# Kernel tuning notes

Measured on AMD Instinct MI355X. Metric: run time of the kernel, lower is better.

The kernel has to match this reference:

```python
import jax, jax.numpy as jnp
import numpy as np

B, I, H, OH = 16384, 256, 256, 64
N_STEPS = 8  # fixed-step dopri5 (adaptive step control replaced by fixed grid for jit)


def setup_inputs() -> dict:
    key = jax.random.key(0)
    ks = jax.random.split(key, 12)
    sH = 1.0 / np.sqrt(H)
    sOH = 1.0 / np.sqrt(OH)
    u = lambda k, shape, s: jax.random.uniform(k, shape, jnp.float32, -s, s)
    return {
        "input": jax.random.normal(ks[0], (B, I), jnp.float32),
        "h_prev": jax.random.normal(ks[1], (B, H), jnp.float32),
        "c_prev": jax.random.normal(ks[2], (B, H), jnp.float32),
        "timespans": jax.random.uniform(ks[3], (B,), jnp.float32, 0.05, 1.0),
        # LSTMCell params (PyTorch layout: gates stacked as [i, f, g, o])
        "W_ih": u(ks[4], (4 * H, I), sH),
        "W_hh": u(ks[5], (4 * H, H), sH),
        "b_ih": u(ks[6], (4 * H,), sH),
        "b_hh": u(ks[7], (4 * H,), sH),
        # ode_func: Linear(H, OH) -> Tanh -> Linear(OH, H)
        "W1": u(ks[8], (OH, H), sH),
        "b1": u(ks[9], (OH,), sH),
        "W2": u(ks[10], (H, OH), sOH),
        "b2": u(ks[11], (H,), sOH),
    }


def reference(input, h_prev, c_prev, timespans, W_ih, W_hh, b_ih, b_hh, W1, b1, W2, b2):
    # --- LSTMCell ---
    gates = input @ W_ih.T + b_ih + h_prev @ W_hh.T + b_hh  # (B, 4H)
    gi, gf, gg, go = jnp.split(gates, 4, axis=-1)
    i = jax.nn.sigmoid(gi)
    f = jax.nn.sigmoid(gf)
    g = jnp.tanh(gg)
    o = jax.nn.sigmoid(go)
    c = f * c_prev + i * g
    h = o * jnp.tanh(c)

    # --- Neural ODE: dy/dt = MLP(y), autonomous, Dormand-Prince RK45 ---
    def ode_f(y):
        return jnp.tanh(y @ W1.T + b1) @ W2.T + b2

    dt = (timespans / N_STEPS)[:, None]  # (B, 1) per-sample step size

    def dopri5_step(y, _):
        k1 = ode_f(y)
        k2 = ode_f(y + dt * (1.0 / 5.0 * k1))
        k3 = ode_f(y + dt * (3.0 / 40.0 * k1 + 9.0 / 40.0 * k2))
        k4 = ode_f(y + dt * (44.0 / 45.0 * k1 - 56.0 / 15.0 * k2 + 32.0 / 9.0 * k3))
        k5 = ode_f(y + dt * (19372.0 / 6561.0 * k1 - 25360.0 / 2187.0 * k2
                             + 64448.0 / 6561.0 * k3 - 212.0 / 729.0 * k4))
        k6 = ode_f(y + dt * (9017.0 / 3168.0 * k1 - 355.0 / 33.0 * k2
                             + 46732.0 / 5247.0 * k3 + 49.0 / 176.0 * k4
                             - 5103.0 / 18656.0 * k5))
        y_next = y + dt * (35.0 / 384.0 * k1 + 500.0 / 1113.0 * k3 + 125.0 / 192.0 * k4
                           - 2187.0 / 6784.0 * k5 + 11.0 / 84.0 * k6)
        return y_next, None

    h_ode, _ = jax.lax.scan(dopri5_step, h, None, length=N_STEPS)
    return h_ode, c
```

## Files before the change

### kernel.cpp

```cpp
#include <hip/hip_runtime.h>
#include <hip/hip_bf16.h>


#define B_N 16384
#define H_N 256

typedef __attribute__((ext_vector_type(8))) short short8;
typedef __attribute__((ext_vector_type(4))) unsigned short u16x4;
typedef __attribute__((ext_vector_type(4))) float f32x4;

__device__ __forceinline__ unsigned short f2bf_s(float x) {
  __hip_bfloat16 h = __float2bfloat16(x);
  return *reinterpret_cast<unsigned short*>(&h);
}

__device__ __forceinline__ short8 pack8f(const float* p) {
  const f32x4 a = *(const f32x4*)p;
  const f32x4 b = *(const f32x4*)(p + 4);
  short8 r;
  r[0] = (short)f2bf_s(a[0]); r[1] = (short)f2bf_s(a[1]);
  r[2] = (short)f2bf_s(a[2]); r[3] = (short)f2bf_s(a[3]);
  r[4] = (short)f2bf_s(b[0]); r[5] = (short)f2bf_s(b[1]);
  r[6] = (short)f2bf_s(b[2]); r[7] = (short)f2bf_s(b[3]);
  return r;
}

__device__ __forceinline__ short8 pack8v(f32x4 a, f32x4 b) {
  short8 r;
  r[0] = (short)f2bf_s(a[0]); r[1] = (short)f2bf_s(a[1]);
  r[2] = (short)f2bf_s(a[2]); r[3] = (short)f2bf_s(a[3]);
  r[4] = (short)f2bf_s(b[0]); r[5] = (short)f2bf_s(b[1]);
  r[6] = (short)f2bf_s(b[2]); r[7] = (short)f2bf_s(b[3]);
  return r;
}

__device__ __forceinline__ float fast_sigmoid(float x) {
  return __builtin_amdgcn_rcpf(1.f + __expf(-x));
}
__device__ __forceinline__ float fast_tanh(float x) {
  float e = __expf(2.f * x);
  return 1.f - 2.f * __builtin_amdgcn_rcpf(e + 1.f);
}

__device__ __forceinline__ void gl_lds16(const void* g, void* l) {
  __builtin_amdgcn_global_load_lds(
      (const __attribute__((address_space(1))) void*)g,
      (__attribute__((address_space(3))) void*)l, 16, 0, 0);
}

__global__ __launch_bounds__(256) void prep_kernel(
    const float* __restrict__ Wih, const float* __restrict__ Whh,
    const float* __restrict__ W1, const float* __restrict__ W2,
    const float* __restrict__ b2,
    unsigned short* __restrict__ wsB, unsigned short* __restrict__ wcB,
    float* __restrict__ uF, unsigned short* __restrict__ w1B,
    unsigned short* __restrict__ w2B) {
  const int bx = blockIdx.x;
  if (bx < 256) {
    int idx = bx * 256 + threadIdx.x;
    int n = idx >> 6, c = idx & 63, k = c * 8;
    const float* src = (k < 256) ? (Wih + (size_t)n * 256 + k)
                                 : (Whh + (size_t)n * 256 + (k - 256));
    *(short8*)(wsB + (size_t)n * 512 + k) = pack8f(src);
  } else if (bx < 272) {
    int idx = (bx - 256) * 256 + threadIdx.x;
    int f = idx >> 6, o = idx & 63;
    float a0 = 0.f, a1 = 0.f, a2 = 0.f, a3 = 0.f;
    for (int h = 0; h < 256; h += 4) {
      a0 = fmaf(W1[f * 256 + h],     W2[h * 64 + o],        a0);
      a1 = fmaf(W1[f * 256 + h + 1], W2[(h + 1) * 64 + o],  a1);
      a2 = fmaf(W1[f * 256 + h + 2], W2[(h + 2) * 64 + o],  a2);
      a3 = fmaf(W1[f * 256 + h + 3], W2[(h + 3) * 64 + o],  a3);
    }
    wcB[f * 64 + o] = f2bf_s((a0 + a1) + (a2 + a3));
  } else if (bx == 272) {
    int f = threadIdx.x;
    if (f < 64) {
      float a0 = 0.f, a1 = 0.f, a2 = 0.f, a3 = 0.f;
      for (int h = 0; h < 256; h += 4) {
        a0 = fmaf(W1[f * 256 + h],     b2[h],     a0);
        a1 = fmaf(W1[f * 256 + h + 1], b2[h + 1], a1);
        a2 = fmaf(W1[f * 256 + h + 2], b2[h + 2], a2);
        a3 = fmaf(W1[f * 256 + h + 3], b2[h + 3], a3);
      }
      uF[f] = (a0 + a1) + (a2 + a3);
    }
  } else if (bx < 281) {
    int idx = (bx - 273) * 256 + threadIdx.x;
    *(short8*)(w1B + (size_t)idx * 8) = pack8f(W1 + (size_t)idx * 8);
  } else {
    int idx = (bx - 281) * 256 + threadIdx.x;
    *(short8*)(w2B + (size_t)idx * 8) = pack8f(W2 + (size_t)idx * 8);
  }
}

__global__ __launch_bounds__(512, 4) void lstm_kernel(
    const float* __restrict__ x, const float* __restrict__ hp,
    const float* __restrict__ cp, const unsigned short* __restrict__ wsB,
    const float* __restrict__ bih, const float* __restrict__ bhh,
    float* __restrict__ out) {
  __shared__ __align__(16) float As2[2][128 * 32];
  __shared__ __align__(16) unsigned short Bs2[2][256 * 32];

  const int tid = threadIdx.x;
  const int lane = tid & 63;
  const int wv = tid >> 6;
  const int rg = wv >> 1;
  const int cg = wv & 1;
  const int s = lane & 15, q = lane >> 4;
  const int mb = blockIdx.x * 128;
  const int hb = blockIdx.y * 64;

  f32x4 acc[2][8];
#pragma unroll
  for (int mt = 0; mt < 2; ++mt)
#pragma unroll
    for (int tn = 0; tn < 8; ++tn) acc[mt][tn] = (f32x4){0.f, 0.f, 0.f, 0.f};

  const int c16a = wv * 2;
  const int rowA0 = c16a * 8 + (lane >> 3);
  const int gcA = (lane & 7) ^ (rowA0 & 7);
  const int rowB0 = c16a * 16 + (lane >> 2);
  const int rowB1 = rowB0 + 16;
  const int gcB0 = (lane & 3) ^ ((rowB0 >> 1) & 3);
  const int gcB1 = (lane & 3) ^ ((rowB1 >> 1) & 3);
  const int grB0 = (rowB0 >> 6) * 256 + hb + (rowB0 & 63);
  const int grB1 = (rowB1 >> 6) * 256 + hb + (rowB1 & 63);

  auto STAGE = [&](int buf, int kt) {
    const float* srcA = (kt < 8) ? x : hp;
    const int kl = (kt * 32) & 255;
    gl_lds16(srcA + (size_t)(mb + rowA0) * 256 + kl + gcA * 4,
             (char*)As2[buf] + c16a * 1024);
    gl_lds16(srcA + (size_t)(mb + rowA0 + 8) * 256 + kl + gcA * 4,
             (char*)As2[buf] + (c16a + 1) * 1024);
    gl_lds16(wsB + (size_t)grB0 * 512 + kt * 32 + gcB0 * 8,
             (char*)Bs2[buf] + c16a * 1024);
    gl_lds16(wsB + (size_t)grB1 * 512 + kt * 32 + gcB1 * 8,
             (char*)Bs2[buf] + (c16a + 1) * 1024);
  };

  STAGE(0, 0);
  __syncthreads();

  for (int kt = 0; kt < 16; ++kt) {
    const int buf = kt & 1;
    if (kt < 15) STAGE(buf ^ 1, kt + 1);

    short8 af[2];
#pragma unroll
    for (int mt = 0; mt < 2; ++mt) {
      const int ar = rg * 32 + mt * 16 + s;
      const char* ap = (const char*)As2[buf] + ar * 128;
      float tmp[8];
      *(f32x4*)tmp = *(const f32x4*)(ap + (((q * 2) ^ (ar & 7)) << 4));
      *(f32x4*)(tmp + 4) = *(const f32x4*)(ap + (((q * 2 + 1) ^ (ar & 7)) << 4));
      af[mt] = pack8f(tmp);
    }
    const char* bp = (const char*)Bs2[buf];
#pragma unroll
    for (int tn = 0; tn < 8; ++tn) {
      const int t = (tn >> 1) * 64 + cg * 32 + (tn & 1) * 16 + s;
      short8 bfr = *(const short8*)(bp + t * 64 + ((q ^ ((t >> 1) & 3)) << 4));
      acc[0][tn] = __builtin_amdgcn_mfma_f32_16x16x32_bf16(af[0], bfr, acc[0][tn], 0, 0, 0);
      acc[1][tn] = __builtin_amdgcn_mfma_f32_16x16x32_bf16(af[1], bfr, acc[1][tn], 0, 0, 0);
    }
    __syncthreads();
  }

#pragma unroll
  for (int mt = 0; mt < 2; ++mt)
#pragma unroll
    for (int ntl = 0; ntl < 2; ++ntl)
#pragma unroll
      for (int r = 0; r < 4; ++r) {
        int sample = mb + rg * 32 + mt * 16 + q * 4 + r;
        int h = hb + cg * 32 + ntl * 16 + s;
        float gi = acc[mt][0 + ntl][r] + bih[h] + bhh[h];
        float gf = acc[mt][2 + ntl][r] + bih[256 + h] + bhh[256 + h];
        float gg = acc[mt][4 + ntl][r] + bih[512 + h] + bhh[512 + h];
        float go = acc[mt][6 + ntl][r] + bih[768 + h] + bhh[768 + h];
        float iv = fast_sigmoid(gi), fv = fast_sigmoid(gf);
        float gv = fast_tanh(gg), ov = fast_sigmoid(go);
        float c = fv * cp[(size_t)sample * 256 + h] + iv * gv;
        float hv = ov * fast_tanh(c);
        out[(size_t)B_N * H_N + (size_t)sample * 256 + h] = c;
        out[(size_t)sample * 256 + h] = hv;
      }
}

__global__ __launch_bounds__(64) void ode_kernel(
    float* __restrict__ out, const float* __restrict__ ts,
    const unsigned short* __restrict__ wcB, const float* __restrict__ uF,
    const unsigned short* __restrict__ w1B, const unsigned short* __restrict__ w2B,
    const float* __restrict__ b1, const float* __restrict__ b2) {
  const int lane = threadIdx.x;
  const int s = lane & 15, q = lane >> 4;
  const int bb = blockIdx.x * 16;

  auto grow = [&](int i) {
    return (i >> 1) * 32 + ((s >> 2) * 8) + (i & 1) * 4 + (s & 3);
  };
  auto fbase = [&](int i) { return (i >> 1) * 32 + q * 8 + (i & 1) * 4; };

  short8 wcf[4][2];
#pragma unroll
  for (int i = 0; i < 4; ++i) {
    const int gr = grow(i);
#pragma unroll
    for (int kt = 0; kt < 2; ++kt)
      wcf[i][kt] = *(const short8*)(wcB + (size_t)gr * 64 + kt * 32 + q * 8);
  }
  f32x4 b1v[4], u4[4];
#pragma unroll
  for (int i = 0; i < 4; ++i) {
    b1v[i] = *(const f32x4*)(b1 + fbase(i));
    u4[i] = *(const f32x4*)(uF + fbase(i));
  }
  const float dt = ts[bb + s] * 0.125f;

  f32x4 G[4];
#pragma unroll
  for (int i = 0; i < 4; ++i) G[i] = (f32x4){0.f, 0.f, 0.f, 0.f};
#pragma unroll
  for (int kt = 0; kt < 8; ++kt) {
    short8 yf = pack8f(out + (size_t)(bb + s) * 256 + kt * 32 + q * 8);
#pragma unroll
    for (int i = 0; i < 4; ++i) {
      short8 w1f =
          *(const short8*)(w1B + (size_t)grow(i) * 256 + kt * 32 + q * 8);
      G[i] = __builtin_amdgcn_mfma_f32_16x16x32_bf16(w1f, yf, G[i], 0, 0, 0);
    }
  }

  auto wcmm = [&](const f32x4 (&zc)[4], f32x4 (&o)[4]) {
    short8 zf0 = pack8v(zc[0], zc[1]);
    short8 zf1 = pack8v(zc[2], zc[3]);
#pragma unroll
    for (int i = 0; i < 4; ++i) {
      f32x4 a = (f32x4){0.f, 0.f, 0.f, 0.f};
      a = __builtin_amdgcn_mfma_f32_16x16x32_bf16(wcf[i][0], zf0, a, 0, 0, 0);
      a = __builtin_amdgcn_mfma_f32_16x16x32_bf16(wcf[i][1], zf1, a, 0, 0, 0);
      o[i] = a;
    }
  };
  auto stage = [&](const f32x4 (&zc)[4], float cj, f32x4 (&zo)[4]) {
    f32x4 o[4];
    wcmm(zc, o);
#pragma unroll
    for (int i = 0; i < 4; ++i)
#pragma unroll
      for (int r = 0; r < 4; ++r)
        zo[i][r] =
            fast_tanh(fmaf(dt, fmaf(cj, u4[i][r], o[i][r]), G[i][r]) + b1v[i][r]);
  };

  const float A31 = 3.f / 40.f, A32 = 9.f / 40.f;
  const float A41 = 44.f / 45.f, A42 = -56.f / 15.f, A43 = 32.f / 9.f;
  const float A51 = 19372.f / 6561.f, A52 = -25360.f / 2187.f,
              A53 = 64448.f / 6561.f, A54 = -212.f / 729.f;
  const float A61 = 9017.f / 3168.f, A62 = -355.f / 33.f, A63 = 46732.f / 5247.f,
              A64 = 49.f / 176.f, A65 = -5103.f / 18656.f;
  const float C1 = 35.f / 384.f, C3 = 500.f / 1113.f, C4 = 125.f / 192.f,
              C5 = -2187.f / 6784.f, C6 = 11.f / 84.f;

  f32x4 SC[4];
#pragma unroll
  for (int i = 0; i < 4; ++i) SC[i] = (f32x4){0.f, 0.f, 0.f, 0.f};
  f32x4 z1[4], z2[4], z3[4], z4[4], z5[4], zc[4];

  for (int st = 0; st < 8; ++st) {
#pragma unroll
    for (int i = 0; i < 4; ++i)
#pragma unroll
      for (int r = 0; r < 4; ++r) z1[i][r] = fast_tanh(G[i][r] + b1v[i][r]);

#pragma unroll
    for (int i = 0; i < 4; ++i) zc[i] = 0.2f * z1[i];
    stage(zc, 0.2f, z2);
#pragma unroll
    for (int i = 0; i < 4; ++i) zc[i] = A31 * z1[i] + A32 * z2[i];
    stage(zc, 0.3f, z3);
#pragma unroll
    for (int i = 0; i < 4; ++i) zc[i] = A41 * z1[i] + A42 * z2[i] + A43 * z3[i];
    stage(zc, 0.8f, z4);
#pragma unroll
    for (int i = 0; i < 4; ++i)
      zc[i] = A51 * z1[i] + A52 * z2[i] + A53 * z3[i] + A54 * z4[i];
    stage(zc, 8.f / 9.f, z5);
#pragma unroll
    for (int i = 0; i < 4; ++i)
      zc[i] = A61 * z1[i] + A62 * z2[i] + A63 * z3[i] + A64 * z4[i] + A65 * z5[i];
    {
      f32x4 o[4];
      wcmm(zc, o);
#pragma unroll
      for (int i = 0; i < 4; ++i)
#pragma unroll
        for (int r = 0; r < 4; ++r) {
          float z6v =
              fast_tanh(fmaf(dt, u4[i][r] + o[i][r], G[i][r]) + b1v[i][r]);
          zc[i][r] = C1 * z1[i][r] + C3 * z3[i][r] + C4 * z4[i][r] +
                     C5 * z5[i][r] + C6 * z6v;
        }
    }
    {
      f32x4 o6[4];
      wcmm(zc, o6);
#pragma unroll
      for (int i = 0; i < 4; ++i) {
        SC[i] += zc[i];
#pragma unroll
        for (int r = 0; r < 4; ++r)
          G[i][r] = fmaf(dt, u4[i][r] + o6[i][r], G[i][r]);
      }
    }
  }

  {
    short8 sf0 = pack8v(SC[0], SC[1]);
    short8 sf1 = pack8v(SC[2], SC[3]);
#pragma unroll
    for (int ft = 0; ft < 16; ++ft) {
      short8 w2a = *(const short8*)(w2B + (size_t)(ft * 16 + s) * 64 + q * 8);
      short8 w2b = *(const short8*)(w2B + (size_t)(ft * 16 + s) * 64 + 32 + q * 8);
      f32x4 a = (f32x4){0.f, 0.f, 0.f, 0.f};
      a = __builtin_amdgcn_mfma_f32_16x16x32_bf16(w2a, sf0, a, 0, 0, 0);
      a = __builtin_amdgcn_mfma_f32_16x16x32_bf16(w2b, sf1, a, 0, 0, 0);
      f32x4 y0 = *(const f32x4*)(out + (size_t)(bb + s) * 256 + ft * 16 + q * 4);
      f32x4 b2v = *(const f32x4*)(b2 + ft * 16 + q * 4);
#pragma unroll
      for (int r = 0; r < 4; ++r)
        y0[r] = fmaf(dt, fmaf(8.f, b2v[r], a[r]), y0[r]);
      *(f32x4*)(out + (size_t)(bb + s) * 256 + ft * 16 + q * 4) = y0;
    }
  }
}

extern "C" void kernel_launch(void* const* d_in, const int* in_sizes, int n_in,
                              void* d_out, int out_size, void* d_ws, size_t ws_size,
                              hipStream_t stream) {
  const float* x   = (const float*)d_in[0];
  const float* hp  = (const float*)d_in[1];
  const float* cp  = (const float*)d_in[2];
  const float* ts  = (const float*)d_in[3];
  const float* Wih = (const float*)d_in[4];
  const float* Whh = (const float*)d_in[5];
  const float* bih = (const float*)d_in[6];
  const float* bhh = (const float*)d_in[7];
  const float* W1  = (const float*)d_in[8];
  const float* b1  = (const float*)d_in[9];
  const float* W2  = (const float*)d_in[10];
  const float* b2  = (const float*)d_in[11];
  float* out = (float*)d_out;

  unsigned short* wsB = (unsigned short*)d_ws;
  unsigned short* wcB = (unsigned short*)((char*)d_ws + 1048576);
  float* uF = (float*)((char*)d_ws + 1048576 + 8192);
  unsigned short* w1B = (unsigned short*)((char*)d_ws + 1048576 + 16384);
  unsigned short* w2B = (unsigned short*)((char*)d_ws + 1048576 + 49152);

  prep_kernel<<<289, 256, 0, stream>>>(Wih, Whh, W1, W2, b2, wsB, wcB, uF, w1B, w2B);
  lstm_kernel<<<dim3(128, 4), 512, 0, stream>>>(x, hp, cp, wsB, bih, bhh, out);
  ode_kernel<<<1024, 64, 0, stream>>>(out, ts, wcB, uF, w1B, w2B, b1, b2);
}
```

Measured before the change: 80.73 us.

## Drop LDS staging in LSTM GEMM and halve ODE samples per wave

The LSTM GEMM no longer stages tiles through LDS with double buffering. Each wave now loads A and B fragments straight from global memory and holds a 64x32 tile across all four gates, so the grid shrinks to 256 blocks. The ODE kernel processes 8 samples per 64-lane wave instead of 16, using clamped duplicate lanes and a masked store, which doubles the block count. It also folds b1 into G once rather than adding it in every stage. The trade-off is more redundant global traffic and duplicated MFMA work in exchange for more parallelism and fewer syncs.

```diff
diff --git a/kernel.cpp b/kernel.cpp
--- a/kernel.cpp
+++ b/kernel.cpp
@@ -40,12 +40,6 @@
 __device__ __forceinline__ float fast_tanh(float x) {
   float e = __expf(2.f * x);
   return 1.f - 2.f * __builtin_amdgcn_rcpf(e + 1.f);
-}
-
-__device__ __forceinline__ void gl_lds16(const void* g, void* l) {
-  __builtin_amdgcn_global_load_lds(
-      (const __attribute__((address_space(1))) void*)g,
-      (__attribute__((address_space(3))) void*)l, 16, 0, 0);
 }
 
 __global__ __launch_bounds__(256) void prep_kernel(
@@ -94,92 +88,54 @@
   }
 }
 
-__global__ __launch_bounds__(512, 4) void lstm_kernel(
+__global__ __launch_bounds__(512, 2) void lstm_kernel(
     const float* __restrict__ x, const float* __restrict__ hp,
     const float* __restrict__ cp, const unsigned short* __restrict__ wsB,
     const float* __restrict__ bih, const float* __restrict__ bhh,
     float* __restrict__ out) {
-  __shared__ __align__(16) float As2[2][128 * 32];
-  __shared__ __align__(16) unsigned short Bs2[2][256 * 32];
-
   const int tid = threadIdx.x;
   const int lane = tid & 63;
   const int wv = tid >> 6;
-  const int rg = wv >> 1;
-  const int cg = wv & 1;
   const int s = lane & 15, q = lane >> 4;
-  const int mb = blockIdx.x * 128;
-  const int hb = blockIdx.y * 64;
-
-  f32x4 acc[2][8];
-#pragma unroll
-  for (int mt = 0; mt < 2; ++mt)
+  const int mb = blockIdx.x * 64;
+  const int hb = wv * 32;
+
+  f32x4 acc[4][8];
+#pragma unroll
+  for (int mt = 0; mt < 4; ++mt)
 #pragma unroll
     for (int tn = 0; tn < 8; ++tn) acc[mt][tn] = (f32x4){0.f, 0.f, 0.f, 0.f};
 
-  const int c16a = wv * 2;
-  const int rowA0 = c16a * 8 + (lane >> 3);
-  const int gcA = (lane & 7) ^ (rowA0 & 7);
-  const int rowB0 = c16a * 16 + (lane >> 2);
-  const int rowB1 = rowB0 + 16;
-  const int gcB0 = (lane & 3) ^ ((rowB0 >> 1) & 3);
-  const int gcB1 = (lane & 3) ^ ((rowB1 >> 1) & 3);
-  const int grB0 = (rowB0 >> 6) * 256 + hb + (rowB0 & 63);
-  const int grB1 = (rowB1 >> 6) * 256 + hb + (rowB1 & 63);
-
-  auto STAGE = [&](int buf, int kt) {
+  for (int kt = 0; kt < 16; ++kt) {
     const float* srcA = (kt < 8) ? x : hp;
     const int kl = (kt * 32) & 255;
-    gl_lds16(srcA + (size_t)(mb + rowA0) * 256 + kl + gcA * 4,
-             (char*)As2[buf] + c16a * 1024);
-    gl_lds16(srcA + (size_t)(mb + rowA0 + 8) * 256 + kl + gcA * 4,
-             (char*)As2[buf] + (c16a + 1) * 1024);
-    gl_lds16(wsB + (size_t)grB0 * 512 + kt * 32 + gcB0 * 8,
-             (char*)Bs2[buf] + c16a * 1024);
-    gl_lds16(wsB + (size_t)grB1 * 512 + kt * 32 + gcB1 * 8,
-             (char*)Bs2[buf] + (c16a + 1) * 1024);
-  };
-
-  STAGE(0, 0);
-  __syncthreads();
-
-  for (int kt = 0; kt < 16; ++kt) {
-    const int buf = kt & 1;
-    if (kt < 15) STAGE(buf ^ 1, kt + 1);
-
-    short8 af[2];
-#pragma unroll
-    for (int mt = 0; mt < 2; ++mt) {
-      const int ar = rg * 32 + mt * 16 + s;
-      const char* ap = (const char*)As2[buf] + ar * 128;
-      float tmp[8];
-      *(f32x4*)tmp = *(const f32x4*)(ap + (((q * 2) ^ (ar & 7)) << 4));
-      *(f32x4*)(tmp + 4) = *(const f32x4*)(ap + (((q * 2 + 1) ^ (ar & 7)) << 4));
-      af[mt] = pack8f(tmp);
-    }
-    const char* bp = (const char*)Bs2[buf];
+    short8 af[4];
+#pragma unroll
+    for (int mt = 0; mt < 4; ++mt)
+      af[mt] = pack8f(srcA + (size_t)(mb + mt * 16 + s) * 256 + kl + q * 8);
 #pragma unroll
     for (int tn = 0; tn < 8; ++tn) {
-      const int t = (tn >> 1) * 64 + cg * 32 + (tn & 1) * 16 + s;
-      short8 bfr = *(const short8*)(bp + t * 64 + ((q ^ ((t >> 1) & 3)) << 4));
-      acc[0][tn] = __builtin_amdgcn_mfma_f32_16x16x32_bf16(af[0], bfr, acc[0][tn], 0, 0, 0);
-      acc[1][tn] = __builtin_amdgcn_mfma_f32_16x16x32_bf16(af[1], bfr, acc[1][tn], 0, 0, 0);
-    }
-    __syncthreads();
-  }
-
-#pragma unroll
-  for (int mt = 0; mt < 2; ++mt)
-#pragma unroll
-    for (int ntl = 0; ntl < 2; ++ntl)
+      const int t = (tn >> 1) * 256 + hb + (tn & 1) * 16 + s;
+      short8 bfr = *(const short8*)(wsB + (size_t)t * 512 + kt * 32 + q * 8);
+#pragma unroll
+      for (int mt = 0; mt < 4; ++mt)
+        acc[mt][tn] =
+            __builtin_amdgcn_mfma_f32_16x16x32_bf16(af[mt], bfr, acc[mt][tn], 0, 0, 0);
+    }
+  }
+
+#pragma unroll
+  for (int mt = 0; mt < 4; ++mt)
+#pragma unroll
+    for (int hsub = 0; hsub < 2; ++hsub)
 #pragma unroll
       for (int r = 0; r < 4; ++r) {
-        int sample = mb + rg * 32 + mt * 16 + q * 4 + r;
-        int h = hb + cg * 32 + ntl * 16 + s;
-        float gi = acc[mt][0 + ntl][r] + bih[h] + bhh[h];
-        float gf = acc[mt][2 + ntl][r] + bih[256 + h] + bhh[256 + h];
-        float gg = acc[mt][4 + ntl][r] + bih[512 + h] + bhh[512 + h];
-        float go = acc[mt][6 + ntl][r] + bih[768 + h] + bhh[768 + h];
+        int sample = mb + mt * 16 + q * 4 + r;
+        int h = hb + hsub * 16 + s;
+        float gi = acc[mt][0 + hsub][r] + bih[h] + bhh[h];
+        float gf = acc[mt][2 + hsub][r] + bih[256 + h] + bhh[256 + h];
+        float gg = acc[mt][4 + hsub][r] + bih[512 + h] + bhh[512 + h];
+        float go = acc[mt][6 + hsub][r] + bih[768 + h] + bhh[768 + h];
         float iv = fast_sigmoid(gi), fv = fast_sigmoid(gf);
         float gv = fast_tanh(gg), ov = fast_sigmoid(go);
         float c = fv * cp[(size_t)sample * 256 + h] + iv * gv;
@@ -196,7 +152,9 @@
     const float* __restrict__ b1, const float* __restrict__ b2) {
   const int lane = threadIdx.x;
   const int s = lane & 15, q = lane >> 4;
-  const int bb = blockIdx.x * 16;
+  const int bb = blockIdx.x * 8;
+  const int sc = (s < 8) ? s : 7;
+  const bool live = (s < 8);
 
   auto grow = [&](int i) {
     return (i >> 1) * 32 + ((s >> 2) * 8) + (i & 1) * 4 + (s & 3);
@@ -217,14 +175,14 @@
     b1v[i] = *(const f32x4*)(b1 + fbase(i));
     u4[i] = *(const f32x4*)(uF + fbase(i));
   }
-  const float dt = ts[bb + s] * 0.125f;
+  const float dt = ts[bb + sc] * 0.125f;
 
   f32x4 G[4];
 #pragma unroll
   for (int i = 0; i < 4; ++i) G[i] = (f32x4){0.f, 0.f, 0.f, 0.f};
 #pragma unroll
   for (int kt = 0; kt < 8; ++kt) {
-    short8 yf = pack8f(out + (size_t)(bb + s) * 256 + kt * 32 + q * 8);
+    short8 yf = pack8f(out + (size_t)(bb + sc) * 256 + kt * 32 + q * 8);
 #pragma unroll
     for (int i = 0; i < 4; ++i) {
       short8 w1f =
@@ -232,6 +190,8 @@
       G[i] = __builtin_amdgcn_mfma_f32_16x16x32_bf16(w1f, yf, G[i], 0, 0, 0);
     }
   }
+#pragma unroll
+  for (int i = 0; i < 4; ++i) G[i] += b1v[i];
 
   auto wcmm = [&](const f32x4 (&zc)[4], f32x4 (&o)[4]) {
     short8 zf0 = pack8v(zc[0], zc[1]);
@@ -251,8 +211,7 @@
     for (int i = 0; i < 4; ++i)
 #pragma unroll
       for (int r = 0; r < 4; ++r)
-        zo[i][r] =
-            fast_tanh(fmaf(dt, fmaf(cj, u4[i][r], o[i][r]), G[i][r]) + b1v[i][r]);
+        zo[i][r] = fast_tanh(fmaf(dt, fmaf(cj, u4[i][r], o[i][r]), G[i][r]));
   };
 
   const float A31 = 3.f / 40.f, A32 = 9.f / 40.f;
@@ -273,7 +232,7 @@
 #pragma unroll
     for (int i = 0; i < 4; ++i)
 #pragma unroll
-      for (int r = 0; r < 4; ++r) z1[i][r] = fast_tanh(G[i][r] + b1v[i][r]);
+      for (int r = 0; r < 4; ++r) z1[i][r] = fast_tanh(G[i][r]);
 
 #pragma unroll
     for (int i = 0; i < 4; ++i) zc[i] = 0.2f * z1[i];
@@ -298,8 +257,7 @@
       for (int i = 0; i < 4; ++i)
 #pragma unroll
         for (int r = 0; r < 4; ++r) {
-          float z6v =
-              fast_tanh(fmaf(dt, u4[i][r] + o[i][r], G[i][r]) + b1v[i][r]);
+          float z6v = fast_tanh(fmaf(dt, u4[i][r] + o[i][r], G[i][r]));
           zc[i][r] = C1 * z1[i][r] + C3 * z3[i][r] + C4 * z4[i][r] +
                      C5 * z5[i][r] + C6 * z6v;
         }
@@ -327,12 +285,13 @@
       f32x4 a = (f32x4){0.f, 0.f, 0.f, 0.f};
       a = __builtin_amdgcn_mfma_f32_16x16x32_bf16(w2a, sf0, a, 0, 0, 0);
       a = __builtin_amdgcn_mfma_f32_16x16x32_bf16(w2b, sf1, a, 0, 0, 0);
-      f32x4 y0 = *(const f32x4*)(out + (size_t)(bb + s) * 256 + ft * 16 + q * 4);
+      f32x4 y0 = *(const f32x4*)(out + (size_t)(bb + sc) * 256 + ft * 16 + q * 4);
       f32x4 b2v = *(const f32x4*)(b2 + ft * 16 + q * 4);
 #pragma unroll
       for (int r = 0; r < 4; ++r)
         y0[r] = fmaf(dt, fmaf(8.f, b2v[r], a[r]), y0[r]);
-      *(f32x4*)(out + (size_t)(bb + s) * 256 + ft * 16 + q * 4) = y0;
+      if (live)
+        *(f32x4*)(out + (size_t)(bb + s) * 256 + ft * 16 + q * 4) = y0;
     }
   }
 }
@@ -361,6 +320,6 @@
   unsigned short* w2B = (unsigned short*)((char*)d_ws + 1048576 + 49152);
 
   prep_kernel<<<289, 256, 0, stream>>>(Wih, Whh, W1, W2, b2, wsB, wcB, uF, w1B, w2B);
-  lstm_kernel<<<dim3(128, 4), 512, 0, stream>>>(x, hp, cp, wsB, bih, bhh, out);
-  ode_kernel<<<1024, 64, 0, stream>>>(out, ts, wcB, uF, w1B, w2B, b1, b2);
-}
+  lstm_kernel<<<256, 512, 0, stream>>>(x, hp, cp, wsB, bih, bhh, out);
+  ode_kernel<<<2048, 64, 0, stream>>>(out, ts, wcB, uF, w1B, w2B, b1, b2);
+}
```

New measurement: 141.2 us. 74.9% more time.
